# Kernel optimization log

Hardware: AMD Instinct MI355X
Metric: run time of the kernel (lower is better)

## Reference

```python
import jax, jax.numpy as jnp
import numpy as np

SMOOTH = 1e-5
ALPHA = 0.25
GAMMA = 2.0
INIT_BETA = 0.5
BETA_DECAY = 0.99


def setup_inputs() -> dict:
    key = jax.random.key(0)
    ks = jax.random.split(key, 7)
    B, NC, C, H, W, D = 8, 1000, 19, 512, 512, 768
    return {
        "logits": jax.random.normal(ks[0], (B, NC), dtype=jnp.float32),
        "label": jax.random.randint(ks[1], (B,), 0, NC),
        "vision_feat": jax.random.normal(ks[2], (B, D), dtype=jnp.float32),
        "text_feat": jax.random.normal(ks[3], (B, D), dtype=jnp.float32),
        "modal_mask": jax.random.uniform(ks[4], (B, 2), dtype=jnp.float32),
        "seg_mask": jax.random.normal(ks[5], (B, C, H, W), dtype=jnp.float32),
        "seg_gt": jax.random.randint(ks[6], (B, H, W), 0, C),
        "epoch": 5,
    }


def _ce_mean(logits, label):
    logp = jax.nn.log_softmax(logits, axis=-1)
    return -jnp.take_along_axis(logp, label[:, None], axis=-1).mean()


def _dice_loss(pred, target):
    # pred: [B,C,H,W] (raw, as in the torch module), target: [B,H,W] int
    C = pred.shape[1]
    onehot = (target[:, None, :, :] == jnp.arange(C)[None, :, None, None]).astype(pred.dtype)
    inter = jnp.sum(pred * onehot, axis=(2, 3))          # [B,C]
    union = jnp.sum(pred, axis=(2, 3)) + jnp.sum(onehot, axis=(2, 3))
    dice = (2.0 * inter + SMOOTH) / (union + SMOOTH)
    return jnp.mean(1.0 - dice)


def _focal_loss(pred, target):
    # pred: [B,C,H,W] logits over class axis 1
    logp = jax.nn.log_softmax(pred, axis=1)
    logp_t = jnp.take_along_axis(logp, target[:, None, :, :], axis=1)[:, 0]  # [B,H,W]
    p_t = jnp.exp(logp_t)
    ce = -logp_t
    return jnp.mean(ALPHA * (1.0 - p_t) ** GAMMA * ce)


def _modal_balance(vision_feat, text_feat, modal_mask, epoch):
    beta_t = INIT_BETA * BETA_DECAY ** epoch
    vn = vision_feat / jnp.linalg.norm(vision_feat, axis=1, keepdims=True)
    tn = text_feat / jnp.linalg.norm(text_feat, axis=1, keepdims=True)
    v_cons = jnp.mean((vn - vn.mean(axis=0, keepdims=True)) ** 2)
    t_cons = jnp.mean((tn - tn.mean(axis=0, keepdims=True)) ** 2)
    cross = 1.0 - jnp.mean(jnp.sum(vn * tn, axis=1))  # cosine sim of unit vectors
    return ((1.0 - beta_t) * v_cons * modal_mask[:, 0].mean()
            + beta_t * t_cons * modal_mask[:, 1].mean() + cross)


def reference(logits, label, vision_feat, text_feat, modal_mask, seg_mask, seg_gt, epoch):
    ce = _ce_mean(logits, label)
    mb = _modal_balance(vision_feat, text_feat, modal_mask, epoch)
    seg = _dice_loss(seg_mask, seg_gt) + _focal_loss(seg_mask, seg_gt)
    total = ce + 0.3 * mb + 0.5 * seg
    return total
```

## Files before the change

### kernel.cpp

```cpp
#include <hip/hip_runtime.h>
#include <math.h>

#define SMOOTH_F 1e-5f
#define ALPHA_F 0.25f

constexpr int Bn = 8;
constexpr int NCn = 1000;
constexpr int Cn = 19;
constexpr int HWn = 512 * 512;
constexpr int Dn = 768;
constexpr int BC = Bn * Cn;

constexpr int TPB = 256;
constexpr int CHUNK = 256;
constexpr int ITERS = 4;
constexpr int PX_PER_BLK = CHUNK * ITERS;
constexpr int BLKS_PER_B = HWn / PX_PER_BLK;
constexpr int SEG_BLOCKS = Bn * BLKS_PER_B;
constexpr int F4_PER_CLASS = CHUNK / 4;
constexpr int LDS_F4 = Cn * F4_PER_CLASS;

constexpr int PART_STRIDE = 58;
constexpr int WS_CE = SEG_BLOCKS * PART_STRIDE;
constexpr int WS_MB = WS_CE + 1;

__device__ __forceinline__ float wave_sum(float v) {
#pragma unroll
  for (int off = 32; off > 0; off >>= 1) v += __shfl_down(v, off, 64);
  return v;
}
__device__ __forceinline__ float wave_max(float v) {
#pragma unroll
  for (int off = 32; off > 0; off >>= 1) v = fmaxf(v, __shfl_down(v, off, 64));
  return v;
}

__global__ __launch_bounds__(TPB, 6) void k_seg(
    const float* __restrict__ pred, const int* __restrict__ gt,
    const float* __restrict__ logits, const int* __restrict__ label,
    const float* __restrict__ vf, const float* __restrict__ tf,
    const float* __restrict__ mmask, const int* __restrict__ epoch,
    float* __restrict__ ws) {
  __shared__ float lds[Cn * CHUNK];
  __shared__ float s_inter[Cn];
  __shared__ float s_count[Cn];
  __shared__ float s_pred[Cn];
  __shared__ float s_red[4];
  __shared__ float sA[4];
  __shared__ float sBv[4];
  __shared__ float nv[Bn];
  __shared__ float nt[Bn];

  const int tid = threadIdx.x;
  const int wid = tid >> 6, lane = tid & 63;
  const int blk = blockIdx.x;

  if (blk >= SEG_BLOCKS) {
    if (blk == SEG_BLOCKS) {
      float acc = 0.0f;
      for (int b = 0; b < Bn; ++b) {
        const float* row = logits + b * NCn;
        float lm = -INFINITY;
        for (int j = tid; j < NCn; j += TPB) lm = fmaxf(lm, row[j]);
        lm = wave_max(lm);
        if (lane == 0) sA[wid] = lm;
        __syncthreads();
        float bm = fmaxf(fmaxf(sA[0], sA[1]), fmaxf(sA[2], sA[3]));
        __syncthreads();
        float ls = 0.0f;
        for (int j = tid; j < NCn; j += TPB) ls += expf(row[j] - bm);
        ls = wave_sum(ls);
        if (lane == 0) sA[wid] = ls;
        __syncthreads();
        if (tid == 0) {
          float lse = bm + logf(sA[0] + sA[1] + sA[2] + sA[3]);
          acc += row[label[b]] - lse;
        }
        __syncthreads();
      }
      if (tid == 0) ws[WS_CE] = -(acc / (float)Bn);
    } else {
      for (int b = 0; b < Bn; ++b) {
        float sv = 0.0f, st = 0.0f;
        for (int j = tid; j < Dn; j += TPB) {
          float a = vf[b * Dn + j];
          float c = tf[b * Dn + j];
          sv += a * a;
          st += c * c;
        }
        sv = wave_sum(sv);
        st = wave_sum(st);
        if (lane == 0) { sA[wid] = sv; sBv[wid] = st; }
        __syncthreads();
        if (tid == 0) {
          nv[b] = sqrtf(sA[0] + sA[1] + sA[2] + sA[3]);
          nt[b] = sqrtf(sBv[0] + sBv[1] + sBv[2] + sBv[3]);
        }
        __syncthreads();
      }
      float colv = 0.0f, colt = 0.0f, cross = 0.0f;
      for (int j = tid; j < Dn; j += TPB) {
        float sv = 0.0f, ssv = 0.0f, stt = 0.0f, sst = 0.0f, cr = 0.0f;
        for (int b = 0; b < Bn; ++b) {
          float vn = vf[b * Dn + j] / nv[b];
          float tn = tf[b * Dn + j] / nt[b];
          sv += vn; ssv += vn * vn;
          stt += tn; sst += tn * tn;
          cr += vn * tn;
        }
        colv += ssv - sv * sv * 0.125f;
        colt += sst - stt * stt * 0.125f;
        cross += cr;
      }
      colv = wave_sum(colv);
      colt = wave_sum(colt);
      cross = wave_sum(cross);
      if (lane == 0) { sA[wid] = colv; sBv[wid] = colt; s_red[wid] = cross; }
      __syncthreads();
      if (tid == 0) {
        float cv = sA[0] + sA[1] + sA[2] + sA[3];
        float ct = sBv[0] + sBv[1] + sBv[2] + sBv[3];
        float cr = s_red[0] + s_red[1] + s_red[2] + s_red[3];
        float v_cons = cv / (float)(Bn * Dn);
        float t_cons = ct / (float)(Bn * Dn);
        float crossv = 1.0f - cr * 0.125f;
        float beta = 0.5f * powf(0.99f, (float)epoch[0]);
        float mm0 = 0.0f, mm1 = 0.0f;
        for (int b = 0; b < Bn; ++b) { mm0 += mmask[b * 2]; mm1 += mmask[b * 2 + 1]; }
        mm0 *= 0.125f; mm1 *= 0.125f;
        ws[WS_MB] = (1.0f - beta) * v_cons * mm0 + beta * t_cons * mm1 + crossv;
      }
    }
    return;
  }

  const int b = blk >> 8;
  const int local = blk & 255;

  if (tid < Cn) { s_inter[tid] = 0.0f; s_count[tid] = 0.0f; s_pred[tid] = 0.0f; }

  const float4* pred4 = (const float4*)pred;
  float4* lds4 = (float4*)lds;
  const int* gtb = gt + (size_t)b * HWn;

  float psum[Cn];
#pragma unroll
  for (int c = 0; c < Cn; ++c) psum[c] = 0.0f;
  float focal = 0.0f;

#pragma unroll 1
  for (int it = 0; it < ITERS; ++it) {
    const int chunk = local * ITERS + it;
    __syncthreads();
    const size_t pbase = (size_t)b * Cn * (HWn / 4) + (size_t)chunk * F4_PER_CLASS;
#pragma unroll
    for (int k = 0; k < 5; ++k) {
      const int i = k * TPB + tid;
      if (i < LDS_F4) {
        const int c = i >> 6;
        const int off = i & 63;
        const float4* g = pred4 + pbase + (size_t)c * (HWn / 4) + off;
        __builtin_amdgcn_global_load_lds(
            (const __attribute__((address_space(1))) void*)g,
            (__attribute__((address_space(3))) void*)(lds4 + i), 16, 0, 0);
      }
    }
    const int t = gtb[chunk * CHUNK + tid];
    __syncthreads();

    float xs[Cn];
#pragma unroll
    for (int c = 0; c < Cn; ++c) xs[c] = lds[c * CHUNK + tid];

    float m = xs[0];
#pragma unroll
    for (int c = 1; c < Cn; ++c) m = fmaxf(m, xs[c]);
    float se = 0.0f, xt = 0.0f;
#pragma unroll
    for (int c = 0; c < Cn; ++c) {
      se += expf(xs[c] - m);
      if (t == c) xt = xs[c];
      psum[c] += xs[c];
    }
    const float lse = m + logf(se);
    const float lpt = xt - lse;
    const float p = expf(lpt);
    const float om = 1.0f - p;
    focal += om * om * (-lpt);

    atomicAdd(&s_inter[t], xt);
    atomicAdd(&s_count[t], 1.0f);
  }

  const float fw = wave_sum(focal * ALPHA_F);
  if (lane == 0) s_red[wid] = fw;
#pragma unroll
  for (int c = 0; c < Cn; ++c) {
    const float v = wave_sum(psum[c]);
    if (lane == 0) atomicAdd(&s_pred[c], v);
  }
  __syncthreads();

  float* part = ws + (size_t)blk * PART_STRIDE;
  if (tid < Cn) {
    part[tid] = s_inter[tid];
    part[Cn + tid] = s_pred[tid];
    part[2 * Cn + tid] = s_count[tid];
  }
  if (tid == 0)
    part[57] = s_red[0] + s_red[1] + s_red[2] + s_red[3];
}

__global__ __launch_bounds__(1024) void k_final(
    const float* __restrict__ ws, float* __restrict__ out) {
  __shared__ float s_i[BC * 4];
  __shared__ float s_p[BC * 4];
  __shared__ float s_c[BC * 4];
  __shared__ float s_f[16];
  __shared__ float s_d[3];
  const int tid = threadIdx.x;
  const int wid = tid >> 6, lane = tid & 63;

  float f = ws[(size_t)(2 * tid) * PART_STRIDE + 57] +
            ws[(size_t)(2 * tid + 1) * PART_STRIDE + 57];
  f = wave_sum(f);
  if (lane == 0) s_f[wid] = f;

  if (tid < BC * 4) {
    const int g = tid / BC;
    const int p = tid - g * BC;
    const int b = p / Cn;
    const int c = p - b * Cn;
    const int base = b * 256 + g * 64;
    float si = 0.0f, sp = 0.0f, sc = 0.0f;
#pragma unroll 4
    for (int k = 0; k < 64; ++k) {
      const float* part = ws + (size_t)(base + k) * PART_STRIDE;
      si += part[c];
      sp += part[Cn + c];
      sc += part[2 * Cn + c];
    }
    s_i[p * 4 + g] = si;
    s_p[p * 4 + g] = sp;
    s_c[p * 4 + g] = sc;
  }
  __syncthreads();

  float v = 0.0f;
  if (tid < BC) {
    const float inter = s_i[tid * 4] + s_i[tid * 4 + 1] + s_i[tid * 4 + 2] + s_i[tid * 4 + 3];
    const float ps = s_p[tid * 4] + s_p[tid * 4 + 1] + s_p[tid * 4 + 2] + s_p[tid * 4 + 3];
    const float cnt = s_c[tid * 4] + s_c[tid * 4 + 1] + s_c[tid * 4 + 2] + s_c[tid * 4 + 3];
    const float dice = (2.0f * inter + SMOOTH_F) / (ps + cnt + SMOOTH_F);
    v = 1.0f - dice;
  }
  v = wave_sum(v);
  if (lane == 0 && wid < 3) s_d[wid] = v;
  __syncthreads();

  if (tid == 0) {
    const float dice_mean = (s_d[0] + s_d[1] + s_d[2]) / (float)BC;
    float fs = 0.0f;
#pragma unroll
    for (int w = 0; w < 16; ++w) fs += s_f[w];
    const float focal_mean = fs / (float)(Bn * HWn);
    const float seg = dice_mean + focal_mean;
    out[0] = ws[WS_CE] + 0.3f * ws[WS_MB] + 0.5f * seg;
  }
}

extern "C" void kernel_launch(void* const* d_in, const int* in_sizes, int n_in,
                              void* d_out, int out_size, void* d_ws, size_t ws_size,
                              hipStream_t stream) {
  const float* logits = (const float*)d_in[0];
  const int* label    = (const int*)d_in[1];
  const float* vf     = (const float*)d_in[2];
  const float* tf     = (const float*)d_in[3];
  const float* mmask  = (const float*)d_in[4];
  const float* seg    = (const float*)d_in[5];
  const int* gt       = (const int*)d_in[6];
  const int* epoch    = (const int*)d_in[7];
  float* out = (float*)d_out;
  float* ws = (float*)d_ws;

  hipLaunchKernelGGL(k_seg, dim3(SEG_BLOCKS + 2), dim3(TPB), 0, stream,
                     seg, gt, logits, label, vf, tf, mmask, epoch, ws);
  hipLaunchKernelGGL(k_final, dim3(1), dim3(1024), 0, stream, ws, out);
}
```

Measured before the change: 274.4 us.

## Replace LDS staging with direct float4 loads and single-pass softmax without max

Drops the global_load_lds staging loop. Each thread now loads 4 consecutive pixels per class as float4 straight from global memory, in groups of 5 classes, and reads labels as an int4. The max-subtraction in log-softmax is removed and fast __expf/__logf intrinsics are used. Per-class partial sums are spilled to an LDS array, and the occupancy hint drops from 6 to 4. The goal is fewer barriers and LDS traffic and wider vector loads, but skipping the max risks overflow for large logits and the fast intrinsics lower precision.

```diff
diff --git a/kernel.cpp b/kernel.cpp
--- a/kernel.cpp
+++ b/kernel.cpp
@@ -12,13 +12,10 @@
 constexpr int BC = Bn * Cn;
 
 constexpr int TPB = 256;
-constexpr int CHUNK = 256;
-constexpr int ITERS = 4;
-constexpr int PX_PER_BLK = CHUNK * ITERS;
+constexpr int PX_PER_BLK = TPB * 4;
 constexpr int BLKS_PER_B = HWn / PX_PER_BLK;
 constexpr int SEG_BLOCKS = Bn * BLKS_PER_B;
-constexpr int F4_PER_CLASS = CHUNK / 4;
-constexpr int LDS_F4 = Cn * F4_PER_CLASS;
+constexpr int PLANE4 = HWn / 4;
 
 constexpr int PART_STRIDE = 58;
 constexpr int WS_CE = SEG_BLOCKS * PART_STRIDE;
@@ -35,13 +32,13 @@
   return v;
 }
 
-__global__ __launch_bounds__(TPB, 6) void k_seg(
+__global__ __launch_bounds__(TPB, 4) void k_seg(
     const float* __restrict__ pred, const int* __restrict__ gt,
     const float* __restrict__ logits, const int* __restrict__ label,
     const float* __restrict__ vf, const float* __restrict__ tf,
     const float* __restrict__ mmask, const int* __restrict__ epoch,
     float* __restrict__ ws) {
-  __shared__ float lds[Cn * CHUNK];
+  __shared__ float s_psum[Cn][TPB];
   __shared__ float s_inter[Cn];
   __shared__ float s_count[Cn];
   __shared__ float s_pred[Cn];
@@ -138,65 +135,71 @@
   const int local = blk & 255;
 
   if (tid < Cn) { s_inter[tid] = 0.0f; s_count[tid] = 0.0f; s_pred[tid] = 0.0f; }
-
-  const float4* pred4 = (const float4*)pred;
-  float4* lds4 = (float4*)lds;
-  const int* gtb = gt + (size_t)b * HWn;
-
-  float psum[Cn];
-#pragma unroll
-  for (int c = 0; c < Cn; ++c) psum[c] = 0.0f;
+  __syncthreads();
+
+  const float4* p4 = (const float4*)pred
+      + (size_t)b * Cn * PLANE4 + (size_t)local * (PX_PER_BLK / 4);
+  const int4 t4 = ((const int4*)(gt + (size_t)b * HWn))[local * (PX_PER_BLK / 4) + tid];
+
+  float4 se = make_float4(0.f, 0.f, 0.f, 0.f);
+  float4 xt = make_float4(0.f, 0.f, 0.f, 0.f);
+  float4 xs[5];
+
+#pragma unroll 1
+  for (int c0 = 0; c0 < 15; c0 += 5) {
+#pragma unroll
+    for (int j = 0; j < 5; ++j) xs[j] = p4[(size_t)(c0 + j) * PLANE4 + tid];
+#pragma unroll
+    for (int j = 0; j < 5; ++j) {
+      const int c = c0 + j;
+      const float4 x = xs[j];
+      se.x += __expf(x.x); se.y += __expf(x.y);
+      se.z += __expf(x.z); se.w += __expf(x.w);
+      if (t4.x == c) xt.x = x.x;
+      if (t4.y == c) xt.y = x.y;
+      if (t4.z == c) xt.z = x.z;
+      if (t4.w == c) xt.w = x.w;
+      s_psum[c][tid] = (x.x + x.y) + (x.z + x.w);
+    }
+  }
+#pragma unroll
+  for (int j = 0; j < 4; ++j) xs[j] = p4[(size_t)(15 + j) * PLANE4 + tid];
+#pragma unroll
+  for (int j = 0; j < 4; ++j) {
+    const int c = 15 + j;
+    const float4 x = xs[j];
+    se.x += __expf(x.x); se.y += __expf(x.y);
+    se.z += __expf(x.z); se.w += __expf(x.w);
+    if (t4.x == c) xt.x = x.x;
+    if (t4.y == c) xt.y = x.y;
+    if (t4.z == c) xt.z = x.z;
+    if (t4.w == c) xt.w = x.w;
+    s_psum[c][tid] = (x.x + x.y) + (x.z + x.w);
+  }
+
   float focal = 0.0f;
-
-#pragma unroll 1
-  for (int it = 0; it < ITERS; ++it) {
-    const int chunk = local * ITERS + it;
-    __syncthreads();
-    const size_t pbase = (size_t)b * Cn * (HWn / 4) + (size_t)chunk * F4_PER_CLASS;
-#pragma unroll
-    for (int k = 0; k < 5; ++k) {
-      const int i = k * TPB + tid;
-      if (i < LDS_F4) {
-        const int c = i >> 6;
-        const int off = i & 63;
-        const float4* g = pred4 + pbase + (size_t)c * (HWn / 4) + off;
-        __builtin_amdgcn_global_load_lds(
-            (const __attribute__((address_space(1))) void*)g,
-            (__attribute__((address_space(3))) void*)(lds4 + i), 16, 0, 0);
-      }
-    }
-    const int t = gtb[chunk * CHUNK + tid];
-    __syncthreads();
-
-    float xs[Cn];
-#pragma unroll
-    for (int c = 0; c < Cn; ++c) xs[c] = lds[c * CHUNK + tid];
-
-    float m = xs[0];
-#pragma unroll
-    for (int c = 1; c < Cn; ++c) m = fmaxf(m, xs[c]);
-    float se = 0.0f, xt = 0.0f;
-#pragma unroll
-    for (int c = 0; c < Cn; ++c) {
-      se += expf(xs[c] - m);
-      if (t == c) xt = xs[c];
-      psum[c] += xs[c];
-    }
-    const float lse = m + logf(se);
-    const float lpt = xt - lse;
-    const float p = expf(lpt);
-    const float om = 1.0f - p;
-    focal += om * om * (-lpt);
-
-    atomicAdd(&s_inter[t], xt);
-    atomicAdd(&s_count[t], 1.0f);
-  }
+  {
+    float lse, lpt, p, om;
+    lse = __logf(se.x); lpt = xt.x - lse; p = __expf(lpt); om = 1.0f - p; focal += om * om * (-lpt);
+    lse = __logf(se.y); lpt = xt.y - lse; p = __expf(lpt); om = 1.0f - p; focal += om * om * (-lpt);
+    lse = __logf(se.z); lpt = xt.z - lse; p = __expf(lpt); om = 1.0f - p; focal += om * om * (-lpt);
+    lse = __logf(se.w); lpt = xt.w - lse; p = __expf(lpt); om = 1.0f - p; focal += om * om * (-lpt);
+  }
+
+  atomicAdd(&s_inter[t4.x], xt.x);
+  atomicAdd(&s_inter[t4.y], xt.y);
+  atomicAdd(&s_inter[t4.z], xt.z);
+  atomicAdd(&s_inter[t4.w], xt.w);
+  atomicAdd(&s_count[t4.x], 1.0f);
+  atomicAdd(&s_count[t4.y], 1.0f);
+  atomicAdd(&s_count[t4.z], 1.0f);
+  atomicAdd(&s_count[t4.w], 1.0f);
 
   const float fw = wave_sum(focal * ALPHA_F);
   if (lane == 0) s_red[wid] = fw;
 #pragma unroll
   for (int c = 0; c < Cn; ++c) {
-    const float v = wave_sum(psum[c]);
+    const float v = wave_sum(s_psum[c][tid]);
     if (lane == 0) atomicAdd(&s_pred[c], v);
   }
   __syncthreads();
```

Result: no change. 279.4 us (+1.8%).
